# Kernel tuning notes

Hardware: AMD Instinct MI355X
Metric: run time of the kernel (lower is better)

## Reference

```python
import jax, jax.numpy as jnp
import numpy as np

N = 50000          # nodes
E = 800000         # edges (avg degree 16)
DIN, DH, DOUT = 128, 256, 40


def setup_inputs() -> dict:
    key = jax.random.key(0)
    ks = jax.random.split(key, 6)
    x = jax.random.normal(ks[0], (N, DIN), dtype=jnp.float32)
    edge_index = jax.random.randint(ks[1], (2, E), 0, N, dtype=jnp.int32)
    W1 = jax.random.normal(ks[2], (DIN, DH), dtype=jnp.float32) * (1.0 / np.sqrt(DIN))
    b1 = jnp.zeros((DH,), dtype=jnp.float32)
    W2 = jax.random.normal(ks[3], (DH, DOUT), dtype=jnp.float32) * (1.0 / np.sqrt(DH))
    b2 = jnp.zeros((DOUT,), dtype=jnp.float32)
    return {"x": x, "edge_index": edge_index, "W1": W1, "b1": b1, "W2": W2, "b2": b2}


def gcn_conv(x, src, dst, W, b, n):
    # PyG GCNConv: add self-loops, symmetric normalization D^-1/2 A D^-1/2,
    # dense projection, scatter-sum aggregation, then bias.
    deg = jax.ops.segment_sum(jnp.ones_like(dst, dtype=x.dtype), dst, num_segments=n)
    dinv = jnp.where(deg > 0, jax.lax.rsqrt(deg), 0.0)
    norm = dinv[src] * dinv[dst]          # [E+N]
    h = x @ W                              # [N, dout] dense GEMM
    msg = h[src] * norm[:, None]          # gather + scale, [E+N, dout]
    out = jax.ops.segment_sum(msg, dst, num_segments=n)  # scatter-add
    return out + b


def reference(x, edge_index, W1, b1, W2, b2):
    n = x.shape[0]
    loops = jnp.arange(n, dtype=edge_index.dtype)
    src = jnp.concatenate([edge_index[0], loops])
    dst = jnp.concatenate([edge_index[1], loops])
    h = jax.nn.relu(gcn_conv(x, src, dst, W1, b1, n))
    h = gcn_conv(h, src, dst, W2, b2, n)
    return jax.nn.log_softmax(h, axis=1)
```

## Files before the change

### kernel.cpp

```cpp
#include <hip/hip_runtime.h>
#include <math.h>

#define DIN 128
#define DH 256
#define DOUT 40
#define MLP_ROWS 64

#define BSH 7
#define BNODES 128
#define NBUK 391
#define CAP 4096
#define PART_T 512
#define PART_EPB 8
#define PART_CHUNK (PART_T * PART_EPB)

typedef short short8 __attribute__((ext_vector_type(8)));
typedef float f32x4 __attribute__((ext_vector_type(4)));

__device__ inline unsigned f2bf(float f) {
    unsigned u = __float_as_uint(f);
    return (u + 0x7fffu + ((u >> 16) & 1u)) >> 16;
}
__device__ inline float bflo(unsigned u) { return __uint_as_float(u << 16); }
__device__ inline float bfhi(unsigned u) { return __uint_as_float(u & 0xffff0000u); }


__global__ __launch_bounds__(PART_T) void k_partition(
    const int* __restrict__ src, const int* __restrict__ dst,
    int* __restrict__ gcur, unsigned* __restrict__ raw, int E) {
    __shared__ int hist[NBUK];
    __shared__ int lbase[NBUK];
    int tid = threadIdx.x;
    int base_e = blockIdx.x * PART_CHUNK;

    for (int i = tid; i < NBUK; i += PART_T) hist[i] = 0;
    __syncthreads();

    int s[PART_EPB], d[PART_EPB];
#pragma unroll
    for (int k = 0; k < PART_EPB; ++k) {
        int e = base_e + k * PART_T + tid;
        if (e < E) { s[k] = src[e]; d[k] = dst[e]; }
        else d[k] = -1;
    }
#pragma unroll
    for (int k = 0; k < PART_EPB; ++k)
        if (d[k] >= 0) atomicAdd(&hist[d[k] >> BSH], 1);
    __syncthreads();

    for (int b = tid; b < NBUK; b += PART_T) {
        int c = hist[b];
        lbase[b] = c ? atomicAdd(&gcur[b], c) : 0;
    }
    __syncthreads();
    for (int i = tid; i < NBUK; i += PART_T) hist[i] = 0;
    __syncthreads();

#pragma unroll
    for (int k = 0; k < PART_EPB; ++k) {
        if (d[k] >= 0) {
            int b = d[k] >> BSH;
            int pos = lbase[b] + atomicAdd(&hist[b], 1);
            if (pos < (b + 1) * CAP)
                raw[pos] = ((unsigned)(d[k] & (BNODES - 1)) << 16) | (unsigned)s[k];
        }
    }
}

__global__ __launch_bounds__(256) void k_bucket_csr(
    const unsigned* __restrict__ raw, const int* __restrict__ gcur,
    int* __restrict__ row_ptr, int* __restrict__ row_end,
    float* __restrict__ dinv, unsigned short* __restrict__ esrc, int n) {
    __shared__ int cnt[BNODES];
    __shared__ int scn[BNODES];
    __shared__ int lcur[BNODES];
    int b = blockIdx.x;
    int tid = threadIdx.x;
    int base = b * CAP;
    int size = gcur[b] - base;
    if (size > CAP) size = CAP;

    if (tid < BNODES) cnt[tid] = 0;
    __syncthreads();
    for (int i = tid; i < size; i += 256)
        atomicAdd(&cnt[raw[base + i] >> 16], 1);
    __syncthreads();

    if (tid < BNODES) scn[tid] = (cnt[tid] + 7) & ~7;
    __syncthreads();
    for (int off = 1; off < BNODES; off <<= 1) {
        int v = 0;
        if (tid < BNODES && tid >= off) v = scn[tid - off];
        __syncthreads();
        if (tid < BNODES) scn[tid] += v;
        __syncthreads();
    }
    if (tid < BNODES) {
        int c8 = (cnt[tid] + 7) & ~7;
        int excl = scn[tid] - c8;
        if (excl > CAP) excl = CAP;
        int re = excl + cnt[tid];
        if (re > CAP) re = CAP;
        lcur[tid] = excl;
        int g = b * BNODES + tid;
        if (g < n) {
            row_ptr[g] = base + excl;
            row_end[g] = base + re;
            dinv[g]    = rsqrtf((float)cnt[tid] + 1.0f);
        }
    }
    __syncthreads();
    for (int i = tid; i < size; i += 256) {
        unsigned rec = raw[base + i];
        int pos = atomicAdd(&lcur[rec >> 16], 1);
        if (pos < CAP) esrc[base + pos] = (unsigned short)(rec & 0xffffu);
    }
}

__global__ void k_prep(const float* __restrict__ x, const float* __restrict__ W1,
                       const float* __restrict__ W2, unsigned* __restrict__ xb,
                       unsigned* __restrict__ w1t, unsigned* __restrict__ w2t,
                       int* __restrict__ gcur, int n64) {
    int i = blockIdx.x * blockDim.x + threadIdx.x;
    if (i < n64) {
        float2 v = ((const float2*)x)[i];
        xb[i] = f2bf(v.x) | (f2bf(v.y) << 16);
        return;
    }
    i -= n64;
    if (i < 256 * 64) {
        int c = i >> 6;
        int kk = (i & 63) * 2;
        w1t[i] = f2bf(W1[kk * DH + c]) | (f2bf(W1[(kk + 1) * DH + c]) << 16);
        return;
    }
    i -= 256 * 64;
    if (i < 48 * 128) {
        int col = i >> 7;
        int kk = (i & 127) * 2;
        float a = (col < DOUT) ? W2[kk * DOUT + col] : 0.f;
        float bb = (col < DOUT) ? W2[(kk + 1) * DOUT + col] : 0.f;
        w2t[i] = f2bf(a) | (f2bf(bb) << 16);
        return;
    }
    i -= 48 * 128;
    if (i < NBUK) gcur[i] = i * CAP;
}

__global__ void k_gather_agg1(const uint2* __restrict__ xb2,
                              const unsigned short* __restrict__ esrc,
                              const int* __restrict__ row_ptr, const int* __restrict__ row_end,
                              const float* __restrict__ dinv, uint2* __restrict__ axb2, int n) {
    int wid = (blockIdx.x * blockDim.x + threadIdx.x) >> 6;
    int lane = threadIdx.x & 63;
    int node = wid * 2 + (lane >> 5);
    int hl = lane & 31;
    if (node >= n) return;
    int beg = row_ptr[node], end = row_end[node];
    float dn = dinv[node];
    uint2 sv = xb2[(size_t)node * 32 + hl];
    float ax = dn * bflo(sv.x), ay = dn * bfhi(sv.x);
    float az = dn * bflo(sv.y), aw = dn * bfhi(sv.y);
    int t = beg;
    for (; t + 8 <= end; t += 8) {
        uint4 q = *(const uint4*)(esrc + t);
        int s0 = q.x & 0xffff, s1 = q.x >> 16, s2 = q.y & 0xffff, s3 = q.y >> 16;
        int s4 = q.z & 0xffff, s5 = q.z >> 16, s6 = q.w & 0xffff, s7 = q.w >> 16;
        float w0 = dinv[s0], w1 = dinv[s1], w2 = dinv[s2], w3 = dinv[s3];
        float w4 = dinv[s4], w5 = dinv[s5], w6 = dinv[s6], w7 = dinv[s7];
        uint2 v0 = xb2[(size_t)s0 * 32 + hl], v1 = xb2[(size_t)s1 * 32 + hl];
        uint2 v2 = xb2[(size_t)s2 * 32 + hl], v3 = xb2[(size_t)s3 * 32 + hl];
        uint2 v4 = xb2[(size_t)s4 * 32 + hl], v5 = xb2[(size_t)s5 * 32 + hl];
        uint2 v6 = xb2[(size_t)s6 * 32 + hl], v7 = xb2[(size_t)s7 * 32 + hl];
        ax += w0 * bflo(v0.x) + w1 * bflo(v1.x) + w2 * bflo(v2.x) + w3 * bflo(v3.x)
            + w4 * bflo(v4.x) + w5 * bflo(v5.x) + w6 * bflo(v6.x) + w7 * bflo(v7.x);
        ay += w0 * bfhi(v0.x) + w1 * bfhi(v1.x) + w2 * bfhi(v2.x) + w3 * bfhi(v3.x)
            + w4 * bfhi(v4.x) + w5 * bfhi(v5.x) + w6 * bfhi(v6.x) + w7 * bfhi(v7.x);
        az += w0 * bflo(v0.y) + w1 * bflo(v1.y) + w2 * bflo(v2.y) + w3 * bflo(v3.y)
            + w4 * bflo(v4.y) + w5 * bflo(v5.y) + w6 * bflo(v6.y) + w7 * bflo(v7.y);
        aw += w0 * bfhi(v0.y) + w1 * bfhi(v1.y) + w2 * bfhi(v2.y) + w3 * bfhi(v3.y)
            + w4 * bfhi(v4.y) + w5 * bfhi(v5.y) + w6 * bfhi(v6.y) + w7 * bfhi(v7.y);
    }
    for (; t < end; ++t) {
        int s = esrc[t];
        float w = dinv[s];
        uint2 v = xb2[(size_t)s * 32 + hl];
        ax += w * bflo(v.x); ay += w * bfhi(v.x);
        az += w * bflo(v.y); aw += w * bfhi(v.y);
    }
    ax *= dn; ay *= dn; az *= dn; aw *= dn;
    axb2[(size_t)node * 32 + hl] =
        make_uint2(f2bf(ax) | (f2bf(ay) << 16), f2bf(az) | (f2bf(aw) << 16));
}

__global__ __launch_bounds__(256) void k_mlp_mfma(
    const unsigned short* __restrict__ axb, const unsigned short* __restrict__ w1t,
    const float* __restrict__ b1, const unsigned short* __restrict__ w2t,
    unsigned short* __restrict__ pb, int n) {
    __shared__ __align__(16) char smem[65536];
    const int tid = threadIdx.x;
    const int lane = tid & 63;
    const int wv = tid >> 6;
    const int l15 = lane & 15;
    const int lg = lane >> 4;
    const int blockRow = blockIdx.x * MLP_ROWS;

    for (int i = tid; i < 256 * 16; i += 256) {
        int j = i >> 4, seg = i & 15;
        short8 v = *(const short8*)(w1t + j * 128 + seg * 8);
        *(short8*)(smem + j * 256 + ((seg * 16) ^ ((j & 7) << 4))) = v;
    }

    int arow = blockRow + wv * 16 + l15;
    if (arow >= n) arow = n - 1;
    const unsigned short* axp = axb + (size_t)arow * DIN + lg * 8;
    short8 aF[4];
#pragma unroll
    for (int ks = 0; ks < 4; ++ks) aF[ks] = *(const short8*)(axp + ks * 32);

    __syncthreads();

    f32x4 acc[16];
#pragma unroll
    for (int nt = 0; nt < 16; ++nt) acc[nt] = (f32x4){0.f, 0.f, 0.f, 0.f};
#pragma unroll
    for (int ks = 0; ks < 4; ++ks) {
        int kb = (ks * 32 + lg * 8) * 2;
#pragma unroll
        for (int nt = 0; nt < 16; ++nt) {
            int j = nt * 16 + l15;
            short8 bF = *(const short8*)(smem + j * 256 + (kb ^ ((j & 7) << 4)));
            acc[nt] = __builtin_amdgcn_mfma_f32_16x16x32_bf16(aF[ks], bF, acc[nt], 0, 0, 0);
        }
    }
    __syncthreads();

    unsigned short* s_h = (unsigned short*)smem;
    unsigned short* s_w2 = (unsigned short*)(smem + 33792);

#pragma unroll
    for (int nt = 0; nt < 16; ++nt) {
        int col = nt * 16 + l15;
        float bias = b1[col];
#pragma unroll
        for (int r = 0; r < 4; ++r) {
            int row = wv * 16 + lg * 4 + r;
            float v = fmaxf(acc[nt][r] + bias, 0.f);
            s_h[row * 264 + col] = (unsigned short)f2bf(v);
        }
    }
    for (int i = tid; i < 48 * 32; i += 256) {
        int j = i >> 5, seg = i & 31;
        short8 v = *(const short8*)(w2t + j * 256 + seg * 8);
        *(short8*)(s_w2 + j * 264 + seg * 8) = v;
    }
    __syncthreads();

    f32x4 acc2[3];
#pragma unroll
    for (int t = 0; t < 3; ++t) acc2[t] = (f32x4){0.f, 0.f, 0.f, 0.f};
#pragma unroll
    for (int ks = 0; ks < 8; ++ks) {
        int k = ks * 32 + lg * 8;
        short8 aH = *(const short8*)(s_h + (wv * 16 + l15) * 264 + k);
#pragma unroll
        for (int t = 0; t < 3; ++t) {
            short8 bF = *(const short8*)(s_w2 + (t * 16 + l15) * 264 + k);
            acc2[t] = __builtin_amdgcn_mfma_f32_16x16x32_bf16(aH, bF, acc2[t], 0, 0, 0);
        }
    }
#pragma unroll
    for (int t = 0; t < 3; ++t) {
        int col = t * 16 + l15;
        if (col < DOUT) {
#pragma unroll
            for (int r = 0; r < 4; ++r) {
                int row = blockRow + wv * 16 + lg * 4 + r;
                if (row < n) pb[(size_t)row * DOUT + col] = (unsigned short)f2bf(acc2[t][r]);
            }
        }
    }
}

__global__ void k_gather2_lsm(const unsigned* __restrict__ pbu,
                              const unsigned short* __restrict__ esrc,
                              const int* __restrict__ row_ptr, const int* __restrict__ row_end,
                              const float* __restrict__ dinv, const float* __restrict__ b2,
                              float* __restrict__ out, int n) {
    int wid = (blockIdx.x * blockDim.x + threadIdx.x) >> 6;
    int lane = threadIdx.x & 63;
    int node = wid * 2 + (lane >> 5);
    int hl = lane & 31;
    if (node >= n) return;
    int beg = row_ptr[node], end = row_end[node];
    float dn = dinv[node];
    int cl = (hl < 20) ? hl : 0;
    unsigned pv = pbu[(size_t)node * 20 + cl];
    float accx = dn * bflo(pv);
    float accy = dn * bfhi(pv);
    int t = beg;
    for (; t + 8 <= end; t += 8) {
        uint4 q = *(const uint4*)(esrc + t);
        int s0 = q.x & 0xffff, s1 = q.x >> 16, s2 = q.y & 0xffff, s3 = q.y >> 16;
        int s4 = q.z & 0xffff, s5 = q.z >> 16, s6 = q.w & 0xffff, s7 = q.w >> 16;
        float w0 = dinv[s0], w1 = dinv[s1], w2 = dinv[s2], w3 = dinv[s3];
        float w4 = dinv[s4], w5 = dinv[s5], w6 = dinv[s6], w7 = dinv[s7];
        unsigned p0 = pbu[(size_t)s0 * 20 + cl], p1 = pbu[(size_t)s1 * 20 + cl];
        unsigned p2 = pbu[(size_t)s2 * 20 + cl], p3 = pbu[(size_t)s3 * 20 + cl];
        unsigned p4 = pbu[(size_t)s4 * 20 + cl], p5 = pbu[(size_t)s5 * 20 + cl];
        unsigned p6 = pbu[(size_t)s6 * 20 + cl], p7 = pbu[(size_t)s7 * 20 + cl];
        accx += w0 * bflo(p0) + w1 * bflo(p1) + w2 * bflo(p2) + w3 * bflo(p3)
              + w4 * bflo(p4) + w5 * bflo(p5) + w6 * bflo(p6) + w7 * bflo(p7);
        accy += w0 * bfhi(p0) + w1 * bfhi(p1) + w2 * bfhi(p2) + w3 * bfhi(p3)
              + w4 * bfhi(p4) + w5 * bfhi(p5) + w6 * bfhi(p6) + w7 * bfhi(p7);
    }
    for (; t < end; ++t) {
        int s = esrc[t];
        float w = dinv[s];
        unsigned p = pbu[(size_t)s * 20 + cl];
        accx += w * bflo(p);
        accy += w * bfhi(p);
    }
    float vx = -INFINITY, vy = -INFINITY;
    if (hl < 20) {
        float2 bv = ((const float2*)b2)[hl];
        vx = dn * accx + bv.x;
        vy = dn * accy + bv.y;
    }
    float m = fmaxf(vx, vy);
#pragma unroll
    for (int off = 16; off; off >>= 1) m = fmaxf(m, __shfl_xor(m, off, 32));
    float ex = (hl < 20) ? (expf(vx - m) + expf(vy - m)) : 0.f;
    float ssum = ex;
#pragma unroll
    for (int off = 16; off; off >>= 1) ssum += __shfl_xor(ssum, off, 32);
    float ls = logf(ssum);
    if (hl < 20)
        ((float2*)(out + (size_t)node * DOUT))[hl] = make_float2(vx - m - ls, vy - m - ls);
}

extern "C" void kernel_launch(void* const* d_in, const int* in_sizes, int n_in,
                              void* d_out, int out_size, void* d_ws, size_t ws_size,
                              hipStream_t stream) {
    const float* x  = (const float*)d_in[0];
    const int*   ei = (const int*)d_in[1];
    const float* W1 = (const float*)d_in[2];
    const float* b1 = (const float*)d_in[3];
    const float* W2 = (const float*)d_in[4];
    const float* b2 = (const float*)d_in[5];
    float* out = (float*)d_out;

    int n = in_sizes[0] / DIN;
    int E = in_sizes[1] / 2;
    const int* src = ei;
    const int* dst = ei + E;

    int*            gcur    = (int*)d_ws;
    int*            row_ptr = gcur + 512;
    int*            row_end = row_ptr + n;
    float*          dinv    = (float*)(row_end + n);
    unsigned*       w1t     = (unsigned*)(dinv + n);
    unsigned*       w2t     = w1t + 16384;
    unsigned*       raw     = w2t + 6144;
    unsigned short* esrc    = (unsigned short*)(raw + (size_t)NBUK * CAP);
    unsigned*       xb      = (unsigned*)(esrc + (size_t)NBUK * CAP);
    unsigned*       axb     = xb + (size_t)n * 64;
    unsigned short* pb      = (unsigned short*)xb;

    const int B = 256;
    int part_blocks = (E + PART_CHUNK - 1) / PART_CHUNK;
    int prep_items = n * 64 + 256 * 64 + 48 * 128 + NBUK;
    int npairs = (n + 1) / 2;
    int gath_blocks = (int)(((size_t)npairs * 64 + B - 1) / B);

    k_prep<<<(prep_items + B - 1) / B, B, 0, stream>>>(x, W1, W2, xb, w1t, w2t, gcur, n * 64);
    k_partition<<<part_blocks, PART_T, 0, stream>>>(src, dst, gcur, raw, E);
    k_bucket_csr<<<NBUK, B, 0, stream>>>(raw, gcur, row_ptr, row_end, dinv, esrc, n);
    k_gather_agg1<<<gath_blocks, B, 0, stream>>>(
        (const uint2*)xb, esrc, row_ptr, row_end, dinv, (uint2*)axb, n);
    k_mlp_mfma<<<(n + MLP_ROWS - 1) / MLP_ROWS, B, 0, stream>>>(
        (const unsigned short*)axb, (const unsigned short*)w1t, b1,
        (const unsigned short*)w2t, pb, n);
    k_gather2_lsm<<<gath_blocks, B, 0, stream>>>(
        (const unsigned*)pb, esrc, row_ptr, row_end, dinv, b2, out, n);
}
```

Measured before the change: 118.3 us.

## Prescale source features by dinv to drop per-edge dinv gathers

Folds the source-side D^-1/2 factor into the features before aggregation. For layer 1 it is applied while converting x to bf16, now done inside the bucket CSR kernel. For layer 2 it is applied to the MFMA output rows. Both gather kernels then sum pre-scaled neighbour rows and no longer issue a random dinv load per edge. The cost is that the x conversion moves into k_bucket_csr, which runs 391 blocks, and the bf16 rounding now happens after scaling, which changes numerics slightly.

```diff
diff --git a/kernel.cpp b/kernel.cpp
--- a/kernel.cpp
+++ b/kernel.cpp
@@ -24,110 +24,10 @@
 __device__ inline float bflo(unsigned u) { return __uint_as_float(u << 16); }
 __device__ inline float bfhi(unsigned u) { return __uint_as_float(u & 0xffff0000u); }
 
-
-__global__ __launch_bounds__(PART_T) void k_partition(
-    const int* __restrict__ src, const int* __restrict__ dst,
-    int* __restrict__ gcur, unsigned* __restrict__ raw, int E) {
-    __shared__ int hist[NBUK];
-    __shared__ int lbase[NBUK];
-    int tid = threadIdx.x;
-    int base_e = blockIdx.x * PART_CHUNK;
-
-    for (int i = tid; i < NBUK; i += PART_T) hist[i] = 0;
-    __syncthreads();
-
-    int s[PART_EPB], d[PART_EPB];
-#pragma unroll
-    for (int k = 0; k < PART_EPB; ++k) {
-        int e = base_e + k * PART_T + tid;
-        if (e < E) { s[k] = src[e]; d[k] = dst[e]; }
-        else d[k] = -1;
-    }
-#pragma unroll
-    for (int k = 0; k < PART_EPB; ++k)
-        if (d[k] >= 0) atomicAdd(&hist[d[k] >> BSH], 1);
-    __syncthreads();
-
-    for (int b = tid; b < NBUK; b += PART_T) {
-        int c = hist[b];
-        lbase[b] = c ? atomicAdd(&gcur[b], c) : 0;
-    }
-    __syncthreads();
-    for (int i = tid; i < NBUK; i += PART_T) hist[i] = 0;
-    __syncthreads();
-
-#pragma unroll
-    for (int k = 0; k < PART_EPB; ++k) {
-        if (d[k] >= 0) {
-            int b = d[k] >> BSH;
-            int pos = lbase[b] + atomicAdd(&hist[b], 1);
-            if (pos < (b + 1) * CAP)
-                raw[pos] = ((unsigned)(d[k] & (BNODES - 1)) << 16) | (unsigned)s[k];
-        }
-    }
-}
-
-__global__ __launch_bounds__(256) void k_bucket_csr(
-    const unsigned* __restrict__ raw, const int* __restrict__ gcur,
-    int* __restrict__ row_ptr, int* __restrict__ row_end,
-    float* __restrict__ dinv, unsigned short* __restrict__ esrc, int n) {
-    __shared__ int cnt[BNODES];
-    __shared__ int scn[BNODES];
-    __shared__ int lcur[BNODES];
-    int b = blockIdx.x;
-    int tid = threadIdx.x;
-    int base = b * CAP;
-    int size = gcur[b] - base;
-    if (size > CAP) size = CAP;
-
-    if (tid < BNODES) cnt[tid] = 0;
-    __syncthreads();
-    for (int i = tid; i < size; i += 256)
-        atomicAdd(&cnt[raw[base + i] >> 16], 1);
-    __syncthreads();
-
-    if (tid < BNODES) scn[tid] = (cnt[tid] + 7) & ~7;
-    __syncthreads();
-    for (int off = 1; off < BNODES; off <<= 1) {
-        int v = 0;
-        if (tid < BNODES && tid >= off) v = scn[tid - off];
-        __syncthreads();
-        if (tid < BNODES) scn[tid] += v;
-        __syncthreads();
-    }
-    if (tid < BNODES) {
-        int c8 = (cnt[tid] + 7) & ~7;
-        int excl = scn[tid] - c8;
-        if (excl > CAP) excl = CAP;
-        int re = excl + cnt[tid];
-        if (re > CAP) re = CAP;
-        lcur[tid] = excl;
-        int g = b * BNODES + tid;
-        if (g < n) {
-            row_ptr[g] = base + excl;
-            row_end[g] = base + re;
-            dinv[g]    = rsqrtf((float)cnt[tid] + 1.0f);
-        }
-    }
-    __syncthreads();
-    for (int i = tid; i < size; i += 256) {
-        unsigned rec = raw[base + i];
-        int pos = atomicAdd(&lcur[rec >> 16], 1);
-        if (pos < CAP) esrc[base + pos] = (unsigned short)(rec & 0xffffu);
-    }
-}
-
-__global__ void k_prep(const float* __restrict__ x, const float* __restrict__ W1,
-                       const float* __restrict__ W2, unsigned* __restrict__ xb,
+__global__ void k_prep(const float* __restrict__ W1, const float* __restrict__ W2,
                        unsigned* __restrict__ w1t, unsigned* __restrict__ w2t,
-                       int* __restrict__ gcur, int n64) {
+                       int* __restrict__ gcur) {
     int i = blockIdx.x * blockDim.x + threadIdx.x;
-    if (i < n64) {
-        float2 v = ((const float2*)x)[i];
-        xb[i] = f2bf(v.x) | (f2bf(v.y) << 16);
-        return;
-    }
-    i -= n64;
     if (i < 256 * 64) {
         int c = i >> 6;
         int kk = (i & 63) * 2;
@@ -145,6 +45,112 @@
     }
     i -= 48 * 128;
     if (i < NBUK) gcur[i] = i * CAP;
+}
+
+__global__ __launch_bounds__(PART_T) void k_partition(
+    const int* __restrict__ src, const int* __restrict__ dst,
+    int* __restrict__ gcur, unsigned* __restrict__ raw, int E) {
+    __shared__ int hist[NBUK];
+    __shared__ int lbase[NBUK];
+    int tid = threadIdx.x;
+    int base_e = blockIdx.x * PART_CHUNK;
+
+    for (int i = tid; i < NBUK; i += PART_T) hist[i] = 0;
+    __syncthreads();
+
+    int s[PART_EPB], d[PART_EPB];
+#pragma unroll
+    for (int k = 0; k < PART_EPB; ++k) {
+        int e = base_e + k * PART_T + tid;
+        if (e < E) { s[k] = src[e]; d[k] = dst[e]; }
+        else d[k] = -1;
+    }
+#pragma unroll
+    for (int k = 0; k < PART_EPB; ++k)
+        if (d[k] >= 0) atomicAdd(&hist[d[k] >> BSH], 1);
+    __syncthreads();
+
+    for (int b = tid; b < NBUK; b += PART_T) {
+        int c = hist[b];
+        lbase[b] = c ? atomicAdd(&gcur[b], c) : 0;
+    }
+    __syncthreads();
+    for (int i = tid; i < NBUK; i += PART_T) hist[i] = 0;
+    __syncthreads();
+
+#pragma unroll
+    for (int k = 0; k < PART_EPB; ++k) {
+        if (d[k] >= 0) {
+            int b = d[k] >> BSH;
+            int pos = lbase[b] + atomicAdd(&hist[b], 1);
+            if (pos < (b + 1) * CAP)
+                raw[pos] = ((unsigned)(d[k] & (BNODES - 1)) << 16) | (unsigned)s[k];
+        }
+    }
+}
+
+__global__ __launch_bounds__(256) void k_bucket_csr(
+    const unsigned* __restrict__ raw, const int* __restrict__ gcur,
+    const float* __restrict__ x,
+    int* __restrict__ row_ptr, int* __restrict__ row_end,
+    float* __restrict__ dinv, unsigned short* __restrict__ esrc,
+    unsigned* __restrict__ xb, int n) {
+    __shared__ int cnt[BNODES];
+    __shared__ int scn[BNODES];
+    __shared__ int lcur[BNODES];
+    __shared__ float sdinv[BNODES];
+    int b = blockIdx.x;
+    int tid = threadIdx.x;
+    int base = b * CAP;
+    int size = gcur[b] - base;
+    if (size > CAP) size = CAP;
+
+    if (tid < BNODES) cnt[tid] = 0;
+    __syncthreads();
+    for (int i = tid; i < size; i += 256)
+        atomicAdd(&cnt[raw[base + i] >> 16], 1);
+    __syncthreads();
+
+    if (tid < BNODES) scn[tid] = (cnt[tid] + 7) & ~7;
+    __syncthreads();
+    for (int off = 1; off < BNODES; off <<= 1) {
+        int v = 0;
+        if (tid < BNODES && tid >= off) v = scn[tid - off];
+        __syncthreads();
+        if (tid < BNODES) scn[tid] += v;
+        __syncthreads();
+    }
+    if (tid < BNODES) {
+        int c8 = (cnt[tid] + 7) & ~7;
+        int excl = scn[tid] - c8;
+        if (excl > CAP) excl = CAP;
+        int re = excl + cnt[tid];
+        if (re > CAP) re = CAP;
+        lcur[tid] = excl;
+        float dv = rsqrtf((float)cnt[tid] + 1.0f);
+        sdinv[tid] = dv;
+        int g = b * BNODES + tid;
+        if (g < n) {
+            row_ptr[g] = base + excl;
+            row_end[g] = base + re;
+            dinv[g]    = dv;
+        }
+    }
+    __syncthreads();
+    for (int i = tid; i < size; i += 256) {
+        unsigned rec = raw[base + i];
+        int pos = atomicAdd(&lcur[rec >> 16], 1);
+        if (pos < CAP) esrc[base + pos] = (unsigned short)(rec & 0xffffu);
+    }
+    int nloc = n - b * BNODES;
+    if (nloc > BNODES) nloc = BNODES;
+    for (int i = tid; i < nloc * 64; i += 256) {
+        int local = i >> 6, c = i & 63;
+        int g = b * BNODES + local;
+        float dv = sdinv[local];
+        float2 v = ((const float2*)x)[(size_t)g * 64 + c];
+        xb[(size_t)g * 64 + c] = f2bf(dv * v.x) | (f2bf(dv * v.y) << 16);
+    }
 }
 
 __global__ void k_gather_agg1(const uint2* __restrict__ xb2,
@@ -157,37 +163,34 @@
     int hl = lane & 31;
     if (node >= n) return;
     int beg = row_ptr[node], end = row_end[node];
-    float dn = dinv[node];
     uint2 sv = xb2[(size_t)node * 32 + hl];
-    float ax = dn * bflo(sv.x), ay = dn * bfhi(sv.x);
-    float az = dn * bflo(sv.y), aw = dn * bfhi(sv.y);
+    float ax = bflo(sv.x), ay = bfhi(sv.x);
+    float az = bflo(sv.y), aw = bfhi(sv.y);
     int t = beg;
     for (; t + 8 <= end; t += 8) {
         uint4 q = *(const uint4*)(esrc + t);
         int s0 = q.x & 0xffff, s1 = q.x >> 16, s2 = q.y & 0xffff, s3 = q.y >> 16;
         int s4 = q.z & 0xffff, s5 = q.z >> 16, s6 = q.w & 0xffff, s7 = q.w >> 16;
-        float w0 = dinv[s0], w1 = dinv[s1], w2 = dinv[s2], w3 = dinv[s3];
-        float w4 = dinv[s4], w5 = dinv[s5], w6 = dinv[s6], w7 = dinv[s7];
         uint2 v0 = xb2[(size_t)s0 * 32 + hl], v1 = xb2[(size_t)s1 * 32 + hl];
         uint2 v2 = xb2[(size_t)s2 * 32 + hl], v3 = xb2[(size_t)s3 * 32 + hl];
         uint2 v4 = xb2[(size_t)s4 * 32 + hl], v5 = xb2[(size_t)s5 * 32 + hl];
         uint2 v6 = xb2[(size_t)s6 * 32 + hl], v7 = xb2[(size_t)s7 * 32 + hl];
-        ax += w0 * bflo(v0.x) + w1 * bflo(v1.x) + w2 * bflo(v2.x) + w3 * bflo(v3.x)
-            + w4 * bflo(v4.x) + w5 * bflo(v5.x) + w6 * bflo(v6.x) + w7 * bflo(v7.x);
-        ay += w0 * bfhi(v0.x) + w1 * bfhi(v1.x) + w2 * bfhi(v2.x) + w3 * bfhi(v3.x)
-            + w4 * bfhi(v4.x) + w5 * bfhi(v5.x) + w6 * bfhi(v6.x) + w7 * bfhi(v7.x);
-        az += w0 * bflo(v0.y) + w1 * bflo(v1.y) + w2 * bflo(v2.y) + w3 * bflo(v3.y)
-            + w4 * bflo(v4.y) + w5 * bflo(v5.y) + w6 * bflo(v6.y) + w7 * bflo(v7.y);
-        aw += w0 * bfhi(v0.y) + w1 * bfhi(v1.y) + w2 * bfhi(v2.y) + w3 * bfhi(v3.y)
-            + w4 * bfhi(v4.y) + w5 * bfhi(v5.y) + w6 * bfhi(v6.y) + w7 * bfhi(v7.y);
+        ax += bflo(v0.x) + bflo(v1.x) + bflo(v2.x) + bflo(v3.x)
+            + bflo(v4.x) + bflo(v5.x) + bflo(v6.x) + bflo(v7.x);
+        ay += bfhi(v0.x) + bfhi(v1.x) + bfhi(v2.x) + bfhi(v3.x)
+            + bfhi(v4.x) + bfhi(v5.x) + bfhi(v6.x) + bfhi(v7.x);
+        az += bflo(v0.y) + bflo(v1.y) + bflo(v2.y) + bflo(v3.y)
+            + bflo(v4.y) + bflo(v5.y) + bflo(v6.y) + bflo(v7.y);
+        aw += bfhi(v0.y) + bfhi(v1.y) + bfhi(v2.y) + bfhi(v3.y)
+            + bfhi(v4.y) + bfhi(v5.y) + bfhi(v6.y) + bfhi(v7.y);
     }
     for (; t < end; ++t) {
         int s = esrc[t];
-        float w = dinv[s];
         uint2 v = xb2[(size_t)s * 32 + hl];
-        ax += w * bflo(v.x); ay += w * bfhi(v.x);
-        az += w * bflo(v.y); aw += w * bfhi(v.y);
-    }
+        ax += bflo(v.x); ay += bfhi(v.x);
+        az += bflo(v.y); aw += bfhi(v.y);
+    }
+    float dn = dinv[node];
     ax *= dn; ay *= dn; az *= dn; aw *= dn;
     axb2[(size_t)node * 32 + hl] =
         make_uint2(f2bf(ax) | (f2bf(ay) << 16), f2bf(az) | (f2bf(aw) << 16));
@@ -196,7 +199,7 @@
 __global__ __launch_bounds__(256) void k_mlp_mfma(
     const unsigned short* __restrict__ axb, const unsigned short* __restrict__ w1t,
     const float* __restrict__ b1, const unsigned short* __restrict__ w2t,
-    unsigned short* __restrict__ pb, int n) {
+    const float* __restrict__ dinv, unsigned short* __restrict__ pb, int n) {
     __shared__ __align__(16) char smem[65536];
     const int tid = threadIdx.x;
     const int lane = tid & 63;
@@ -269,6 +272,12 @@
             acc2[t] = __builtin_amdgcn_mfma_f32_16x16x32_bf16(aH, bF, acc2[t], 0, 0, 0);
         }
     }
+    float dnr[4];
+#pragma unroll
+    for (int r = 0; r < 4; ++r) {
+        int row = blockRow + wv * 16 + lg * 4 + r;
+        dnr[r] = (row < n) ? dinv[row] : 0.f;
+    }
 #pragma unroll
     for (int t = 0; t < 3; ++t) {
         int col = t * 16 + l15;
@@ -276,7 +285,8 @@
 #pragma unroll
             for (int r = 0; r < 4; ++r) {
                 int row = blockRow + wv * 16 + lg * 4 + r;
-                if (row < n) pb[(size_t)row * DOUT + col] = (unsigned short)f2bf(acc2[t][r]);
+                if (row < n)
+                    pb[(size_t)row * DOUT + col] = (unsigned short)f2bf(acc2[t][r] * dnr[r]);
             }
         }
     }
@@ -296,30 +306,27 @@
     float dn = dinv[node];
     int cl = (hl < 20) ? hl : 0;
     unsigned pv = pbu[(size_t)node * 20 + cl];
-    float accx = dn * bflo(pv);
-    float accy = dn * bfhi(pv);
+    float accx = bflo(pv);
+    float accy = bfhi(pv);
     int t = beg;
     for (; t + 8 <= end; t += 8) {
         uint4 q = *(const uint4*)(esrc + t);
         int s0 = q.x & 0xffff, s1 = q.x >> 16, s2 = q.y & 0xffff, s3 = q.y >> 16;
         int s4 = q.z & 0xffff, s5 = q.z >> 16, s6 = q.w & 0xffff, s7 = q.w >> 16;
-        float w0 = dinv[s0], w1 = dinv[s1], w2 = dinv[s2], w3 = dinv[s3];
-        float w4 = dinv[s4], w5 = dinv[s5], w6 = dinv[s6], w7 = dinv[s7];
         unsigned p0 = pbu[(size_t)s0 * 20 + cl], p1 = pbu[(size_t)s1 * 20 + cl];
         unsigned p2 = pbu[(size_t)s2 * 20 + cl], p3 = pbu[(size_t)s3 * 20 + cl];
         unsigned p4 = pbu[(size_t)s4 * 20 + cl], p5 = pbu[(size_t)s5 * 20 + cl];
         unsigned p6 = pbu[(size_t)s6 * 20 + cl], p7 = pbu[(size_t)s7 * 20 + cl];
-        accx += w0 * bflo(p0) + w1 * bflo(p1) + w2 * bflo(p2) + w3 * bflo(p3)
-              + w4 * bflo(p4) + w5 * bflo(p5) + w6 * bflo(p6) + w7 * bflo(p7);
-        accy += w0 * bfhi(p0) + w1 * bfhi(p1) + w2 * bfhi(p2) + w3 * bfhi(p3)
-              + w4 * bfhi(p4) + w5 * bfhi(p5) + w6 * bfhi(p6) + w7 * bfhi(p7);
+        accx += bflo(p0) + bflo(p1) + bflo(p2) + bflo(p3)
+              + bflo(p4) + bflo(p5) + bflo(p6) + bflo(p7);
+        accy += bfhi(p0) + bfhi(p1) + bfhi(p2) + bfhi(p3)
+              + bfhi(p4) + bfhi(p5) + bfhi(p6) + bfhi(p7);
     }
     for (; t < end; ++t) {
         int s = esrc[t];
-        float w = dinv[s];
         unsigned p = pbu[(size_t)s * 20 + cl];
-        accx += w * bflo(p);
-        accy += w * bfhi(p);
+        accx += bflo(p);
+        accy += bfhi(p);
     }
     float vx = -INFINITY, vy = -INFINITY;
     if (hl < 20) {
@@ -369,18 +376,18 @@
 
     const int B = 256;
     int part_blocks = (E + PART_CHUNK - 1) / PART_CHUNK;
-    int prep_items = n * 64 + 256 * 64 + 48 * 128 + NBUK;
+    int prep_items = 256 * 64 + 48 * 128 + NBUK;
     int npairs = (n + 1) / 2;
     int gath_blocks = (int)(((size_t)npairs * 64 + B - 1) / B);
 
-    k_prep<<<(prep_items + B - 1) / B, B, 0, stream>>>(x, W1, W2, xb, w1t, w2t, gcur, n * 64);
+    k_prep<<<(prep_items + B - 1) / B, B, 0, stream>>>(W1, W2, w1t, w2t, gcur);
     k_partition<<<part_blocks, PART_T, 0, stream>>>(src, dst, gcur, raw, E);
-    k_bucket_csr<<<NBUK, B, 0, stream>>>(raw, gcur, row_ptr, row_end, dinv, esrc, n);
+    k_bucket_csr<<<NBUK, B, 0, stream>>>(raw, gcur, x, row_ptr, row_end, dinv, esrc, xb, n);
     k_gather_agg1<<<gath_blocks, B, 0, stream>>>(
         (const uint2*)xb, esrc, row_ptr, row_end, dinv, (uint2*)axb, n);
     k_mlp_mfma<<<(n + MLP_ROWS - 1) / MLP_ROWS, B, 0, stream>>>(
         (const unsigned short*)axb, (const unsigned short*)w1t, b1,
-        (const unsigned short*)w2t, pb, n);
+        (const unsigned short*)w2t, dinv, pb, n);
     k_gather2_lsm<<<gath_blocks, B, 0, stream>>>(
         (const unsigned*)pb, esrc, row_ptr, row_end, dinv, b2, out, n);
 }
```

New measurement: 120.9 us. +2.2%, slower.
